# Kernel optimization log

Measured on AMD Instinct MI355X. Metric: run time of the kernel, lower is better.

Reference implementation:

```python
import jax, jax.numpy as jnp
import numpy as np

B, S, D, H, DFF = 8, 1024, 1024, 16, 4096
DK = D // H
EPS = 1e-5


def setup_inputs() -> dict:
    key = jax.random.key(0)
    ks = jax.random.split(key, 12)
    sc = lambda n: 1.0 / np.sqrt(n)
    return {
        "x": jax.random.normal(ks[0], (B, S, D), jnp.float32),
        "src_mask": jnp.ones((B, 1, 1, S), jnp.int32),
        "wq": jax.random.normal(ks[1], (D, D), jnp.float32) * sc(D),
        "bq": jnp.zeros((D,), jnp.float32),
        "wk": jax.random.normal(ks[2], (D, D), jnp.float32) * sc(D),
        "bk": jnp.zeros((D,), jnp.float32),
        "wv": jax.random.normal(ks[3], (D, D), jnp.float32) * sc(D),
        "bv": jnp.zeros((D,), jnp.float32),
        "wo": jax.random.normal(ks[4], (D, D), jnp.float32) * sc(D),
        "bo": jnp.zeros((D,), jnp.float32),
        "w1": jax.random.normal(ks[5], (DFF, D), jnp.float32) * sc(D),
        "b1": jnp.zeros((DFF,), jnp.float32),
        "w2": jax.random.normal(ks[6], (D, DFF), jnp.float32) * sc(DFF),
        "b2": jnp.zeros((D,), jnp.float32),
        "g1": jnp.ones((1,), jnp.float32),
        "be1": jnp.zeros((1,), jnp.float32),
        "g2": jnp.ones((1,), jnp.float32),
        "be2": jnp.zeros((1,), jnp.float32),
    }


def _layernorm(x, gamma, beta):
    # Faithful to source: torch.var defaults to unbiased (ddof=1); scalar gamma/beta.
    mu = jnp.mean(x, axis=-1, keepdims=True)
    var = jnp.var(x, axis=-1, keepdims=True, ddof=1)
    return gamma * (x - mu) / jnp.sqrt(var + EPS) + beta


def _mha(x, wq, bq, wk, bk, wv, bv, wo, bo):
    q = (x @ wq.T + bq).reshape(B, S, H, DK).transpose(0, 2, 1, 3)
    k = (x @ wk.T + bk).reshape(B, S, H, DK).transpose(0, 2, 1, 3)
    v = (x @ wv.T + bv).reshape(B, S, H, DK).transpose(0, 2, 1, 3)
    scores = jnp.einsum("bhqd,bhkd->bhqk", q, k) / np.sqrt(DK)
    # NOTE: source uses non-inplace masked_fill whose result is discarded,
    # so the mask has no effect on the executed math; we replicate that.
    attn = jax.nn.softmax(scores, axis=-1)
    out = jnp.einsum("bhqk,bhkd->bhqd", attn, v)
    out = out.transpose(0, 2, 1, 3).reshape(B, S, D)
    return out @ wo.T + bo


def reference(x, src_mask, wq, bq, wk, bk, wv, bv, wo, bo,
              w1, b1, w2, b2, g1, be1, g2, be2):
    # residual 1: pre-norm self-attention (dropout=0 in eval)
    x = x + _mha(_layernorm(x, g1, be1), wq, bq, wk, bk, wv, bv, wo, bo)
    # residual 2: pre-norm FFN
    h = _layernorm(x, g2, be2)
    ff = jax.nn.relu(h @ w1.T + b1) @ w2.T + b2
    return x + ff
```

## Files before the change

### kernel.cpp

```cpp
#include <hip/hip_runtime.h>

typedef unsigned short u16;
typedef unsigned int u32;
typedef __attribute__((ext_vector_type(8))) __bf16 bf16x8;
typedef __attribute__((ext_vector_type(4))) float f32x4;

#define B_ 8
#define S_ 1024
#define D_ 1024
#define H_ 16
#define DK_ 64
#define DFF_ 4096
#define LDQKV 3072

__device__ __forceinline__ float bflo(u32 u) { return __uint_as_float(u << 16); }
__device__ __forceinline__ float bfhi(u32 u) { return __uint_as_float(u & 0xffff0000u); }
__device__ __forceinline__ u16 f2bf(float f) {
    u32 u = __float_as_uint(f);
    u += 0x7fffu + ((u >> 16) & 1u);
    return (u16)(u >> 16);
}
__device__ __forceinline__ u32 cvtpk(float lo, float hi) {
    u32 r;
    asm("v_cvt_pk_bf16_f32 %0, %1, %2" : "=v"(r) : "v"(lo), "v"(hi));
    return r;
}

__device__ __forceinline__ void gl2lds16(const u16* g, u16* l) {
    __builtin_amdgcn_global_load_lds(
        (const __attribute__((address_space(1))) void*)g,
        (__attribute__((address_space(3))) void*)l, 16, 0, 0);
}

__global__ __launch_bounds__(256) void sniff_kernel(const u16* __restrict__ w,
                                                    int* __restrict__ flag) {
    float mx = 0.f;
    for (int i = threadIdx.x; i < 4096; i += 256) {
        float v = fabsf(bflo((u32)w[i]));
        if (!isnan(v)) mx = fmaxf(mx, v);
    }
#pragma unroll
    for (int m = 1; m < 64; m <<= 1) mx = fmaxf(mx, __shfl_xor(mx, m, 64));
    __shared__ float wmx[4];
    if ((threadIdx.x & 63) == 0) wmx[threadIdx.x >> 6] = mx;
    __syncthreads();
    if (threadIdx.x == 0) {
        float m2 = fmaxf(fmaxf(wmx[0], wmx[1]), fmaxf(wmx[2], wmx[3]));
        *flag = (m2 > 1e3f) ? 1 : 0;
    }
}

__global__ __launch_bounds__(256) void norm_kernel(const void* __restrict__ in,
                                                   u16* __restrict__ out, int n,
                                                   const int* __restrict__ flag) {
    const int i = blockIdx.x * 256 + threadIdx.x;
    if (i >= n) return;
    if (*flag)
        out[i] = f2bf(((const float*)in)[i]);
    else
        out[i] = ((const u16*)in)[i];
}

struct SmallTbl {
    const void* src[10];
    u16* dst[10];
    int n[10];
};
__global__ __launch_bounds__(256) void norm_small(SmallTbl tb,
                                                  const int* __restrict__ flag) {
    int i = blockIdx.x * 256 + threadIdx.x;
    const int f = *flag;
#pragma unroll
    for (int j = 0; j < 10; ++j) {
        if (i < tb.n[j]) {
            if (f)
                tb.dst[j][i] = f2bf(((const float*)tb.src[j])[i]);
            else
                tb.dst[j][i] = ((const u16*)tb.src[j])[i];
            return;
        }
        i -= tb.n[j];
    }
}

template <int INF>
__global__ __launch_bounds__(256) void ln_kernel(const void* __restrict__ in,
                                                 const u16* __restrict__ gs,
                                                 const u16* __restrict__ bs,
                                                 u16* __restrict__ out,
                                                 const int* __restrict__ flag) {
    const int row = blockIdx.x, t = threadIdx.x;
    const bool f32in = (INF == 1) || (INF == 2 && flag[0] != 0);
    float v0, v1, v2, v3;
    if (f32in) {
        const float* p = (const float*)in + (size_t)row * D_ + t * 4;
        float4 f = *(const float4*)p;
        v0 = f.x; v1 = f.y; v2 = f.z; v3 = f.w;
    } else {
        const u16* p = (const u16*)in + (size_t)row * D_ + t * 4;
        uint2 u = *(const uint2*)p;
        v0 = bflo(u.x); v1 = bfhi(u.x); v2 = bflo(u.y); v3 = bfhi(u.y);
    }
    float s = v0 + v1 + v2 + v3;
    float sq = v0 * v0 + v1 * v1 + v2 * v2 + v3 * v3;
#pragma unroll
    for (int m = 1; m < 64; m <<= 1) {
        s += __shfl_xor(s, m, 64);
        sq += __shfl_xor(sq, m, 64);
    }
    __shared__ float ss[4], sqs[4];
    const int w = t >> 6;
    if ((t & 63) == 0) { ss[w] = s; sqs[w] = sq; }
    __syncthreads();
    s = ss[0] + ss[1] + ss[2] + ss[3];
    sq = sqs[0] + sqs[1] + sqs[2] + sqs[3];
    const float mu = s * (1.f / 1024.f);
    float var = (sq - 1024.f * mu * mu) * (1.f / 1023.f);
    var = fmaxf(var, 0.f);
    const float rstd = rsqrtf(var + 1e-5f);
    const float gm = bflo((u32)gs[0]);
    const float bt = bflo((u32)bs[0]);
    const float y0 = gm * (v0 - mu) * rstd + bt;
    const float y1 = gm * (v1 - mu) * rstd + bt;
    const float y2 = gm * (v2 - mu) * rstd + bt;
    const float y3 = gm * (v3 - mu) * rstd + bt;
    uint2 uo;
    uo.x = (u32)f2bf(y0) | ((u32)f2bf(y1) << 16);
    uo.y = (u32)f2bf(y2) | ((u32)f2bf(y3) << 16);
    *(uint2*)(out + (size_t)row * D_ + t * 4) = uo;
}

template <int RELU, int RES, int OUTF>
__global__ __launch_bounds__(256, 4) void gemm_bt(const u16* __restrict__ A,
                                                  const u16* __restrict__ W,
                                                  const u16* __restrict__ bias,
                                                  const void* __restrict__ res,
                                                  void* __restrict__ out,
                                                  int M, int N, int K,
                                                  const int* __restrict__ oflag) {
    __shared__ __align__(16) u16 As[128 * 64];
    __shared__ __align__(16) u16 Bs[128 * 64];
    const int t = threadIdx.x;
    const int lane = t & 63, w = t >> 6;
    const int wm = w >> 1, wn = w & 1;

    const int nx = N >> 7;
    const int gsz = nx << 3;
    const int id = blockIdx.x;
    const int grp = id / gsz;
    const int rem = id - grp * gsz;
    const int m0 = ((grp << 3) + (rem & 7)) << 7;
    const int n0 = (rem >> 3) << 7;

    f32x4 acc[4][4];
#pragma unroll
    for (int mi = 0; mi < 4; ++mi)
#pragma unroll
        for (int ni = 0; ni < 4; ++ni) acc[mi][ni] = (f32x4){0.f, 0.f, 0.f, 0.f};

    const int r8 = lane >> 3, s8 = lane & 7;
    const int cg = s8 ^ r8;
    const u16* Ag = A + (size_t)(m0 + w * 8 + r8) * K + cg * 8;
    const u16* Bg = W + (size_t)(n0 + w * 8 + r8) * K + cg * 8;
    const size_t rI = (size_t)32 * K;
    u16* Asd = &As[(w * 8) * 64];
    u16* Bsd = &Bs[(w * 8) * 64];

    const int c = lane & 15, g = lane >> 4;
    const u16* As_r = &As[(wm * 64 + c) * 64];
    const u16* Bs_r = &Bs[(wn * 64 + c) * 64];
    const int sl0 = (g ^ (c & 7)) * 8;
    const int sl1 = ((4 + g) ^ (c & 7)) * 8;

    for (int kt = 0; kt < K; kt += 64) {
        __syncthreads();
        gl2lds16(Ag, Asd);
        gl2lds16(Ag + rI, Asd + 32 * 64);
        gl2lds16(Ag + 2 * rI, Asd + 64 * 64);
        gl2lds16(Ag + 3 * rI, Asd + 96 * 64);
        gl2lds16(Bg, Bsd);
        gl2lds16(Bg + rI, Bsd + 32 * 64);
        gl2lds16(Bg + 2 * rI, Bsd + 64 * 64);
        gl2lds16(Bg + 3 * rI, Bsd + 96 * 64);
        Ag += 64; Bg += 64;
        __syncthreads();
#pragma unroll
        for (int kc = 0; kc < 2; ++kc) {
            const int sl = kc ? sl1 : sl0;
            bf16x8 af[4], bfr[4];
#pragma unroll
            for (int i = 0; i < 4; ++i) {
                af[i] = *(const bf16x8*)(As_r + i * 16 * 64 + sl);
                bfr[i] = *(const bf16x8*)(Bs_r + i * 16 * 64 + sl);
            }
#pragma unroll
            for (int mi = 0; mi < 4; ++mi)
#pragma unroll
                for (int ni = 0; ni < 4; ++ni)
                    acc[mi][ni] = __builtin_amdgcn_mfma_f32_16x16x32_bf16(af[mi], bfr[ni], acc[mi][ni], 0, 0, 0);
        }
    }

    const int fl = oflag ? oflag[0] : 0;
    const bool f32o = (OUTF == 1) || (OUTF == 2 && fl != 0);
    const int qd = lane >> 4, cl = lane & 15;
#pragma unroll
    for (int ni = 0; ni < 4; ++ni) {
        const int col = n0 + wn * 64 + ni * 16 + cl;
        const float bv = bflo((u32)bias[col]);
#pragma unroll
        for (int mi = 0; mi < 4; ++mi) {
#pragma unroll
            for (int j = 0; j < 4; ++j) {
                const int row = m0 + wm * 64 + mi * 16 + qd * 4 + j;
                float vv = acc[mi][ni][j] + bv;
                if (RELU) vv = fmaxf(vv, 0.f);
                if (RES == 2) vv += ((const float*)res)[(size_t)row * N + col];
                if (RES == 3) {
                    if (fl)
                        vv += ((const float*)res)[(size_t)row * N + col];
                    else
                        vv += bflo((u32)((const u16*)res)[(size_t)row * N + col]);
                }
                if (f32o)
                    ((float*)out)[(size_t)row * N + col] = vv;
                else
                    ((u16*)out)[(size_t)row * N + col] = f2bf(vv);
            }
        }
    }
}

__global__ __launch_bounds__(256, 2) void attn_mfma(const u16* __restrict__ QKV,
                                                    u16* __restrict__ O) {
    __shared__ __align__(16) u16 lds[6 * 64 * 64];
    u16* Ks = lds;
    u16* VsT = lds + 64 * 64;

    const int t = threadIdx.x;
    const int lane = t & 63, w = t >> 6;
    u16* Pw = lds + (2 + w) * 64 * 64;
    const int b = blockIdx.y >> 4, h = blockIdx.y & 15;
    const int q_base = blockIdx.x * 256 + w * 64;
    const int c = lane & 15, g = lane >> 4;
    const int c7 = c & 7;
    const float SC = 0.18033688011112042f;

    bf16x8 qfrag[4][2];
#pragma unroll
    for (int ni = 0; ni < 4; ++ni)
#pragma unroll
        for (int kc = 0; kc < 2; ++kc)
            qfrag[ni][kc] = *(const bf16x8*)(QKV + (size_t)(b * S_ + q_base + 16 * ni + c) * LDQKV +
                                             h * 64 + kc * 32 + 8 * g);

    f32x4 acc_o[4][4];
#pragma unroll
    for (int mi = 0; mi < 4; ++mi)
#pragma unroll
        for (int ni = 0; ni < 4; ++ni) acc_o[mi][ni] = (f32x4){0.f, 0.f, 0.f, 0.f};
    float m_st[4] = {-1e30f, -1e30f, -1e30f, -1e30f};
    float l_st[4] = {0.f, 0.f, 0.f, 0.f};

    const size_t kbase = (size_t)(b * S_) * LDQKV + 1024 + h * 64;
    const size_t vbase = (size_t)(b * S_) * LDQKV + 2048 + h * 64;

    const int r8 = lane >> 3, s8 = lane & 7;
    const int cgk = s8 ^ r8;
    const u16* Kg = QKV + kbase + (size_t)(w * 8 + r8) * LDQKV + cgk * 8;
    u16* Ksd = &Ks[(w * 8) * 64];
    const size_t rIk = (size_t)32 * LDQKV;

    const int vr = t >> 3, vdq = t & 7;
    const u16* Vg = QKV + vbase + (size_t)(2 * vr) * LDQKV + vdq * 8;

    int vfx[4];
#pragma unroll
    for (int mi = 0; mi < 4; ++mi) vfx[mi] = c7 ^ ((2 * mi + (c >> 3)) & 7);

    for (int kt = 0; kt < 16; ++kt) {
        __syncthreads();
        gl2lds16(Kg, Ksd);
        gl2lds16(Kg + rIk, Ksd + 32 * 64);
        Kg += (size_t)64 * LDQKV;
        {
            uint4 a = *(const uint4*)Vg;
            uint4 bb = *(const uint4*)(Vg + LDQKV);
            Vg += (size_t)64 * LDQKV;
            const u32 aw[4] = {a.x, a.y, a.z, a.w};
            const u32 bw[4] = {bb.x, bb.y, bb.z, bb.w};
#pragma unroll
            for (int i = 0; i < 8; ++i) {
                u32 wv;
                if (i & 1)
                    wv = (aw[i >> 1] >> 16) | (bw[i >> 1] & 0xffff0000u);
                else
                    wv = (aw[i >> 1] & 0xffffu) | (bw[i >> 1] << 16);
                const int d = vdq * 8 + i;
                *(u32*)&VsT[d * 64 + (((vr >> 2) ^ (i ^ vdq)) << 3) + ((vr & 3) << 1)] = wv;
            }
        }
        __syncthreads();

        f32x4 acc_s[4][4];
#pragma unroll
        for (int mi = 0; mi < 4; ++mi)
#pragma unroll
            for (int ni = 0; ni < 4; ++ni) acc_s[mi][ni] = (f32x4){0.f, 0.f, 0.f, 0.f};
        __builtin_amdgcn_s_setprio(1);
#pragma unroll
        for (int kc = 0; kc < 2; ++kc) {
            bf16x8 kf[4];
#pragma unroll
            for (int mi = 0; mi < 4; ++mi)
                kf[mi] = *(const bf16x8*)&Ks[(16 * mi + c) * 64 + (((kc * 4 + g) ^ c7) << 3)];
#pragma unroll
            for (int mi = 0; mi < 4; ++mi)
#pragma unroll
                for (int ni = 0; ni < 4; ++ni)
                    acc_s[mi][ni] = __builtin_amdgcn_mfma_f32_16x16x32_bf16(
                        kf[mi], qfrag[ni][kc], acc_s[mi][ni], 0, 0, 0);
        }
        __builtin_amdgcn_s_setprio(0);

        float alpha[4];
        bool resc[4];
#pragma unroll
        for (int ni = 0; ni < 4; ++ni) {
            float mx = -1e30f;
#pragma unroll
            for (int mi = 0; mi < 4; ++mi) {
#pragma unroll
                for (int j = 0; j < 4; ++j) mx = fmaxf(mx, acc_s[mi][ni][j]);
            }
            mx = fmaxf(mx, __shfl_xor(mx, 16, 64));
            mx = fmaxf(mx, __shfl_xor(mx, 32, 64));
            const float mo = m_st[ni];
            const float mn = fmaxf(mo, mx);
            resc[ni] = __any(mn > mo);
            if (resc[ni]) {
                alpha[ni] = exp2f((mo - mn) * SC);
                m_st[ni] = mn;
            } else {
                alpha[ni] = 1.f;
            }
            const float nms = m_st[ni] * SC;
            float sum = 0.f;
#pragma unroll
            for (int mi = 0; mi < 4; ++mi) {
                const float p0 = exp2f(fmaf(acc_s[mi][ni][0], SC, -nms));
                const float p1 = exp2f(fmaf(acc_s[mi][ni][1], SC, -nms));
                const float p2 = exp2f(fmaf(acc_s[mi][ni][2], SC, -nms));
                const float p3 = exp2f(fmaf(acc_s[mi][ni][3], SC, -nms));
                sum += (p0 + p1) + (p2 + p3);
                uint2 pk;
                pk.x = cvtpk(p0, p1);
                pk.y = cvtpk(p2, p3);
                *(uint2*)&Pw[(16 * ni + c) * 64 +
                             ((((2 * mi + (g >> 1)) ^ c7) << 3) + ((g & 1) << 2))] = pk;
            }
            sum += __shfl_xor(sum, 16, 64);
            sum += __shfl_xor(sum, 32, 64);
            l_st[ni] = (resc[ni] ? l_st[ni] * alpha[ni] : l_st[ni]) + sum;
        }
#pragma unroll
        for (int ni = 0; ni < 4; ++ni) {
            if (resc[ni]) {
#pragma unroll
                for (int mi = 0; mi < 4; ++mi) {
#pragma unroll
                    for (int j = 0; j < 4; ++j) acc_o[mi][ni][j] *= alpha[ni];
                }
            }
        }

        __builtin_amdgcn_s_setprio(1);
#pragma unroll
        for (int kc = 0; kc < 2; ++kc) {
            bf16x8 vf[4], pf[4];
#pragma unroll
            for (int mi = 0; mi < 4; ++mi)
                vf[mi] = *(const bf16x8*)&VsT[(16 * mi + c) * 64 + (((kc * 4 + g) ^ vfx[mi]) << 3)];
#pragma unroll
            for (int ni = 0; ni < 4; ++ni)
                pf[ni] = *(const bf16x8*)&Pw[(16 * ni + c) * 64 + (((kc * 4 + g) ^ c7) << 3)];
#pragma unroll
            for (int mi = 0; mi < 4; ++mi)
#pragma unroll
                for (int ni = 0; ni < 4; ++ni)
                    acc_o[mi][ni] = __builtin_amdgcn_mfma_f32_16x16x32_bf16(
                        vf[mi], pf[ni], acc_o[mi][ni], 0, 0, 0);
        }
        __builtin_amdgcn_s_setprio(0);
    }

#pragma unroll
    for (int ni = 0; ni < 4; ++ni) {
        const float inv_l = 1.f / l_st[ni];
        u16* op = O + (size_t)(b * S_ + q_base + 16 * ni + c) * D_ + h * 64;
#pragma unroll
        for (int mi = 0; mi < 4; ++mi) {
            uint2 uo;
            uo.x = cvtpk(acc_o[mi][ni][0] * inv_l, acc_o[mi][ni][1] * inv_l);
            uo.y = cvtpk(acc_o[mi][ni][2] * inv_l, acc_o[mi][ni][3] * inv_l);
            *(uint2*)(op + 16 * mi + 4 * g) = uo;
        }
    }
}

extern "C" void kernel_launch(void* const* d_in, const int* in_sizes, int n_in,
                              void* d_out, int out_size, void* d_ws, size_t ws_size,
                              hipStream_t stream) {
    (void)in_sizes; (void)n_in; (void)out_size; (void)ws_size;
    char* ws = (char*)d_ws;
    const size_t MB = 1ull << 20;
    const size_t KB = 1024;
    u16* wqkv = (u16*)(ws + 16 * MB);
    u16* won  = (u16*)(ws + 22 * MB);
    u16* w1n  = (u16*)(ws + 24 * MB);
    u16* w2n  = (u16*)(ws + 32 * MB);
    u16* bqkv = (u16*)(ws + 40 * MB);
    u16* bon  = (u16*)(ws + 40 * MB + 64 * KB);
    u16* b1n  = (u16*)(ws + 40 * MB + 128 * KB);
    u16* b2n  = (u16*)(ws + 40 * MB + 192 * KB);
    u16* g1n  = (u16*)(ws + 40 * MB + 256 * KB);
    u16* be1n = (u16*)(ws + 40 * MB + 320 * KB);
    u16* g2n  = (u16*)(ws + 40 * MB + 384 * KB);
    u16* be2n = (u16*)(ws + 40 * MB + 448 * KB);
    int* flag = (int*)(ws + 40 * MB + 512 * KB);
    u16* h1   = (u16*)(ws + 48 * MB);
    u16* qkv  = (u16*)(ws + 64 * MB);
    float* x2 = (float*)(ws + 64 * MB);
    u16* h2   = (u16*)(ws + 96 * MB);
    u16* f1   = (u16*)(ws + 112 * MB);

    const int M = B_ * S_;

    sniff_kernel<<<1, 256, 0, stream>>>((const u16*)d_in[2], flag);
    auto nrm = [&](const void* in, u16* out, int n) {
        norm_kernel<<<(n + 255) / 256, 256, 0, stream>>>(in, out, n, flag);
    };
    nrm(d_in[2],  wqkv,               D_ * D_);
    nrm(d_in[4],  wqkv + D_ * D_,     D_ * D_);
    nrm(d_in[6],  wqkv + 2 * D_ * D_, D_ * D_);
    nrm(d_in[8],  won, D_ * D_);
    nrm(d_in[10], w1n, DFF_ * D_);
    nrm(d_in[12], w2n, D_ * DFF_);
    {
        SmallTbl tb;
        tb.src[0] = d_in[3];  tb.dst[0] = bqkv;          tb.n[0] = D_;
        tb.src[1] = d_in[5];  tb.dst[1] = bqkv + D_;     tb.n[1] = D_;
        tb.src[2] = d_in[7];  tb.dst[2] = bqkv + 2 * D_; tb.n[2] = D_;
        tb.src[3] = d_in[9];  tb.dst[3] = bon;           tb.n[3] = D_;
        tb.src[4] = d_in[11]; tb.dst[4] = b1n;           tb.n[4] = DFF_;
        tb.src[5] = d_in[13]; tb.dst[5] = b2n;           tb.n[5] = D_;
        tb.src[6] = d_in[14]; tb.dst[6] = g1n;           tb.n[6] = 1;
        tb.src[7] = d_in[15]; tb.dst[7] = be1n;          tb.n[7] = 1;
        tb.src[8] = d_in[16]; tb.dst[8] = g2n;           tb.n[8] = 1;
        tb.src[9] = d_in[17]; tb.dst[9] = be2n;          tb.n[9] = 1;
        const int tot = 5 * D_ + DFF_ + 4;
        norm_small<<<(tot + 255) / 256, 256, 0, stream>>>(tb, flag);
    }

    ln_kernel<2><<<M, 256, 0, stream>>>(d_in[0], g1n, be1n, h1, flag);
    gemm_bt<0, 0, 0><<<(LDQKV / 128) * (M / 128), 256, 0, stream>>>(h1, wqkv, bqkv, nullptr, qkv, M, LDQKV, D_, flag);
    attn_mfma<<<dim3(S_ / 256, B_ * H_), 256, 0, stream>>>(qkv, h1);
    gemm_bt<0, 3, 1><<<(D_ / 128) * (M / 128), 256, 0, stream>>>(h1, won, bon, d_in[0], x2, M, D_, D_, flag);
    ln_kernel<1><<<M, 256, 0, stream>>>((const void*)x2, g2n, be2n, h2, flag);
    gemm_bt<1, 0, 0><<<(DFF_ / 128) * (M / 128), 256, 0, stream>>>(h2, w1n, b1n, nullptr, f1, M, DFF_, D_, flag);
    gemm_bt<0, 2, 2><<<(D_ / 128) * (M / 128), 256, 0, stream>>>(f1, w2n, b2n, (const void*)x2, (void*)d_out, M, D_, DFF_, flag);
}
```

Measured before the change: 539.7 us.

## Add 256x256-tile 512-thread GEMM for QKV and FFN1 projections

Adds a new bf16 MFMA GEMM kernel using 256x256 output tiles with 8 waves, a double-buffered LDS pipeline staged in K-halves, grouped block ordering for L2 reuse, and s_setprio around the MFMA bursts. It replaces the 128x128 gemm_bt for the QKV projection and the first FFN layer, which have large N. The goal is higher arithmetic intensity and less global/LDS traffic per FLOP. The trade-offs are fewer blocks, heavy register pressure (128 accumulator floats per thread), and the removal of the flag-based dtype handling in those calls.

```diff
diff --git a/kernel.cpp b/kernel.cpp
--- a/kernel.cpp
+++ b/kernel.cpp
@@ -226,6 +226,120 @@
                     ((float*)out)[(size_t)row * N + col] = vv;
                 else
                     ((u16*)out)[(size_t)row * N + col] = f2bf(vv);
+            }
+        }
+    }
+}
+
+template <int RELU>
+__global__ __launch_bounds__(512, 2) void gemm256(const u16* __restrict__ A,
+                                                  const u16* __restrict__ W,
+                                                  const u16* __restrict__ bias,
+                                                  u16* __restrict__ out,
+                                                  int M, int N, int K) {
+    __shared__ __align__(16) u16 As[2][2][256 * 32];
+    __shared__ __align__(16) u16 Bs[2][2][256 * 32];
+    const int t = threadIdx.x;
+    const int lane = t & 63, w = t >> 6;
+    const int wm = w >> 2, wn = w & 3;
+
+    const int nx = N >> 8;
+    const int gsz = nx << 3;
+    const int id = blockIdx.x;
+    const int grp = id / gsz;
+    const int rem = id - grp * gsz;
+    const int m0 = ((grp << 3) + (rem & 7)) << 8;
+    const int n0 = (rem >> 3) << 8;
+
+    f32x4 acc[8][4];
+#pragma unroll
+    for (int mi = 0; mi < 8; ++mi)
+#pragma unroll
+        for (int ni = 0; ni < 4; ++ni) acc[mi][ni] = (f32x4){0.f, 0.f, 0.f, 0.f};
+
+    const int vr = lane >> 2, vs = lane & 3;
+    const int cgs = vs ^ (vr & 3);
+    const u16* Asrc = A + (size_t)(m0 + w * 16 + vr) * K + cgs * 8;
+    const u16* Bsrc = W + (size_t)(n0 + w * 16 + vr) * K + cgs * 8;
+    const size_t rI = (size_t)128 * K;
+
+    auto stageA = [&](int p, int kc, int tk) {
+        u16* d = &As[p][kc][(w * 16) * 32];
+        const u16* s = Asrc + (size_t)tk * 64 + kc * 32;
+        gl2lds16(s, d);
+        gl2lds16(s + rI, d + 128 * 32);
+    };
+    auto stageB = [&](int p, int kc, int tk) {
+        u16* d = &Bs[p][kc][(w * 16) * 32];
+        const u16* s = Bsrc + (size_t)tk * 64 + kc * 32;
+        gl2lds16(s, d);
+        gl2lds16(s + rI, d + 128 * 32);
+    };
+
+    const int c = lane & 15, g = lane >> 4;
+    const int sx = (g ^ (c & 3)) << 3;
+
+    const int nt = K >> 6;
+    stageA(0, 0, 0); stageB(0, 0, 0);
+    stageA(0, 1, 0); stageB(0, 1, 0);
+    stageA(1, 0, 1); stageB(1, 0, 1);
+    asm volatile("s_waitcnt vmcnt(4)" ::: "memory");
+    __builtin_amdgcn_s_barrier();
+    __builtin_amdgcn_sched_barrier(0);
+
+    int cur = 0;
+    for (int kt = 0; kt < nt; ++kt) {
+#pragma unroll
+        for (int ph = 0; ph < 4; ++ph) {
+            const int kc = ph >> 1, qm = ph & 1;
+            bf16x8 af[4], bfv[4];
+            const u16* Ab = &As[cur][kc][0];
+            const u16* Bb = &Bs[cur][kc][0];
+#pragma unroll
+            for (int i = 0; i < 4; ++i)
+                af[i] = *(const bf16x8*)(Ab + (wm * 128 + (qm * 4 + i) * 16 + c) * 32 + sx);
+#pragma unroll
+            for (int i = 0; i < 4; ++i)
+                bfv[i] = *(const bf16x8*)(Bb + (wn * 64 + i * 16 + c) * 32 + sx);
+            if (ph == 0) { if (kt + 1 < nt) stageA(cur ^ 1, 1, kt + 1); }
+            else if (ph == 1) { if (kt + 1 < nt) stageB(cur ^ 1, 1, kt + 1); }
+            else if (ph == 2) { if (kt + 2 < nt) stageA(cur, 0, kt + 2); }
+            else { if (kt + 2 < nt) stageB(cur, 0, kt + 2); }
+            __builtin_amdgcn_s_barrier();
+            __builtin_amdgcn_s_setprio(1);
+#pragma unroll
+            for (int mi = 0; mi < 4; ++mi)
+#pragma unroll
+                for (int ni = 0; ni < 4; ++ni)
+                    acc[qm * 4 + mi][ni] = __builtin_amdgcn_mfma_f32_16x16x32_bf16(
+                        af[mi], bfv[ni], acc[qm * 4 + mi][ni], 0, 0, 0);
+            __builtin_amdgcn_s_setprio(0);
+            if (ph < 3) {
+                __builtin_amdgcn_s_barrier();
+                if (ph == 1) __builtin_amdgcn_sched_barrier(0);
+            }
+        }
+        if (kt < nt - 2)
+            asm volatile("s_waitcnt vmcnt(4)" ::: "memory");
+        else
+            asm volatile("s_waitcnt vmcnt(0)" ::: "memory");
+        __builtin_amdgcn_s_barrier();
+        __builtin_amdgcn_sched_barrier(0);
+        cur ^= 1;
+    }
+
+#pragma unroll
+    for (int ni = 0; ni < 4; ++ni) {
+        const int col = n0 + wn * 64 + ni * 16 + c;
+        const float bv = bflo((u32)bias[col]);
+#pragma unroll
+        for (int mi = 0; mi < 8; ++mi) {
+#pragma unroll
+            for (int j = 0; j < 4; ++j) {
+                const int row = m0 + wm * 128 + mi * 16 + g * 4 + j;
+                float vv = acc[mi][ni][j] + bv;
+                if (RELU) vv = fmaxf(vv, 0.f);
+                out[(size_t)row * N + col] = f2bf(vv);
             }
         }
     }
@@ -463,10 +577,10 @@
     }
 
     ln_kernel<2><<<M, 256, 0, stream>>>(d_in[0], g1n, be1n, h1, flag);
-    gemm_bt<0, 0, 0><<<(LDQKV / 128) * (M / 128), 256, 0, stream>>>(h1, wqkv, bqkv, nullptr, qkv, M, LDQKV, D_, flag);
+    gemm256<0><<<(LDQKV / 256) * (M / 256), 512, 0, stream>>>(h1, wqkv, bqkv, qkv, M, LDQKV, D_);
     attn_mfma<<<dim3(S_ / 256, B_ * H_), 256, 0, stream>>>(qkv, h1);
     gemm_bt<0, 3, 1><<<(D_ / 128) * (M / 128), 256, 0, stream>>>(h1, won, bon, d_in[0], x2, M, D_, D_, flag);
     ln_kernel<1><<<M, 256, 0, stream>>>((const void*)x2, g2n, be2n, h2, flag);
-    gemm_bt<1, 0, 0><<<(DFF_ / 128) * (M / 128), 256, 0, stream>>>(h2, w1n, b1n, nullptr, f1, M, DFF_, D_, flag);
+    gemm256<1><<<(DFF_ / 256) * (M / 256), 512, 0, stream>>>(h2, w1n, b1n, f1, M, DFF_, D_);
     gemm_bt<0, 2, 2><<<(D_ / 128) * (M / 128), 256, 0, stream>>>(f1, w2n, b2n, (const void*)x2, (void*)d_out, M, D_, DFF_, flag);
 }
```

New measurement: 565.2 us. 4.7% more time.
